# Performance work log

Hardware: AMD Instinct MI355X
Metric: run time of the kernel (lower is better)

## Reference

```python
import jax, jax.numpy as jnp
import numpy as np

N_NODES = 50000
N_EDGES = 800000
N_GRAPHS = 256
W_SCALE = 0.05  # keep activations bounded through 5 relu conv layers


def setup_inputs() -> dict:
    key = jax.random.key(0)
    ks = jax.random.split(key, 16)
    rn = lambda k, shape: W_SCALE * jax.random.normal(k, shape, dtype=jnp.float32)
    return {
        "x": jax.random.normal(ks[0], (N_NODES, 336), dtype=jnp.float32),
        "edge_index": jax.random.randint(ks[1], (2, N_EDGES), 0, N_NODES, dtype=jnp.int32),
        "batch": jnp.sort(jax.random.randint(ks[2], (N_NODES,), 0, N_GRAPHS, dtype=jnp.int32)),
        "w1_rel": rn(ks[3], (100, 336)),
        "w1_root": rn(ks[4], (100, 336)),
        "b1": rn(ks[5], (100,)),
        "w_rel": rn(ks[6], (4, 100, 100)),
        "w_root": rn(ks[7], (4, 100, 100)),
        "b": rn(ks[8], (4, 100)),
        "lw1": rn(ks[9], (100, 100)),
        "lb1": rn(ks[10], (100,)),
        "lw2": rn(ks[11], (100, 100)),
        "lb2": rn(ks[12], (100,)),
        "lw3": rn(ks[13], (29, 100)),
        "lb3": rn(ks[14], (29,)),
    }


def _graph_conv(x, edge_index, w_rel, w_root, bias):
    # PyG GraphConv: out_i = W_rel @ (sum_{j->i} x_j) + b + W_root @ x_i
    src, dst = edge_index[0], edge_index[1]
    agg = jax.ops.segment_sum(x[src], dst, num_segments=x.shape[0])  # [N, d_in]
    return agg @ w_rel.T + bias + x @ w_root.T


def reference(x, edge_index, batch, w1_rel, w1_root, b1, w_rel, w_root, b,
              lw1, lb1, lw2, lb2, lw3, lb3):
    h = jax.nn.relu(_graph_conv(x, edge_index, w1_rel, w1_root, b1))  # [N,100]
    for i in range(4):  # conv2..conv5 (structurally distinct params)
        h = jax.nn.relu(_graph_conv(h, edge_index, w_rel[i], w_root[i], b[i]))
    # global_mean_pool over graphs
    sums = jax.ops.segment_sum(h, batch, num_segments=N_GRAPHS)          # [G,100]
    counts = jax.ops.segment_sum(jnp.ones((h.shape[0],), h.dtype), batch,
                                 num_segments=N_GRAPHS)                  # [G]
    pooled = sums / jnp.maximum(counts, 1.0)[:, None]
    h = jax.nn.relu(pooled @ lw1.T + lb1)
    h = jax.nn.relu(h @ lw2.T + lb2)
    return h @ lw3.T + lb3  # [G, 29]
```

## Files before the change

### kernel.cpp

```cpp
#include <hip/hip_runtime.h>

#define N_NODES 50000
#define N_EDGES 800000
#define N_GRAPHS 256
#define F 100

#define SCAN_B 512
#define SCAN_NB 98
#define SCAN_PAD (SCAN_NB * SCAN_B)

#define PART_SZ 6250
#define FILL_CHUNK 2048
#define HIST_BLOCKS 3128

#define SROW 72
#define EPS 264
#define AST 264

#define SENT N_NODES
#define CSR_CAP 1155072

typedef __attribute__((ext_vector_type(8))) short bf16x8;
typedef __attribute__((ext_vector_type(4))) float f32x4;
typedef unsigned short ushort_t;
typedef unsigned int uint_t;

__device__ inline ushort_t f2bf(float f) {
  uint_t u = __float_as_uint(f);
  uint_t r = (u + 0x7fffu + ((u >> 16) & 1u)) >> 16;
  return (ushort_t)r;
}


__global__ __launch_bounds__(256) void pack_all(
    const float* __restrict__ w1_rel, const float* __restrict__ w1_root,
    const float* __restrict__ w_rel, const float* __restrict__ w_root,
    ushort_t* __restrict__ Wp1, ushort_t* __restrict__ Wf, int* __restrict__ cnt,
    int* __restrict__ csr, ushort_t* __restrict__ ZP,
    ushort_t* __restrict__ H1, ushort_t* __restrict__ H2) {
  int b = blockIdx.x;
  int tid = threadIdx.x;
  if (b < 208) {
    int row = b;
    for (int k = tid; k < 384; k += 256) {
      float v = 0.f;
      if (k < 336) {
        if (row < 100) v = w1_rel[row * 336 + k];
        else if (row < 200) v = w1_root[(row - 100) * 336 + k];
      }
      Wp1[(size_t)row * 384 + k] = f2bf(v);
    }
  } else if (b < 720) {
    int rowl = b - 208;
    int l = rowl >> 7, row = rowl & 127;
    int k = tid;
    float v = 0.f;
    if (row < 100) {
      if (k < 100) v = w_rel[((size_t)l * 100 + row) * 100 + k];
      else if (k >= 128 && k < 228) v = w_root[((size_t)l * 100 + row) * 100 + (k - 128)];
    }
    Wf[(size_t)rowl * 256 + k] = f2bf(v);
  } else if (b < 769) {
    int z = b - 720;
    *(int4*)(cnt + (size_t)z * 1024 + tid * 4) = make_int4(0, 0, 0, 0);
  } else if (b < 1051) {
    int i0 = (b - 769) * 4096 + tid * 16;
    int4 sv = make_int4(SENT, SENT, SENT, SENT);
    *(int4*)(csr + i0) = sv; *(int4*)(csr + i0 + 4) = sv;
    *(int4*)(csr + i0 + 8) = sv; *(int4*)(csr + i0 + 12) = sv;
  } else {
    uint4 z4 = make_uint4(0u, 0u, 0u, 0u);
    if (tid < 32)      *(uint4*)(ZP + (size_t)SENT * 256 + tid * 8) = z4;
    else if (tid < 48) *(uint4*)(H1 + (size_t)SENT * 128 + (tid - 32) * 8) = z4;
    else if (tid < 64) *(uint4*)(H2 + (size_t)SENT * 128 + (tid - 48) * 8) = z4;
  }
}


__global__ __launch_bounds__(256) void hist_kernel(const int* __restrict__ dst,
                                                   int* __restrict__ cnt, int E) {
  int part = blockIdx.x & 7;
  int lo = part * PART_SZ, hi = lo + PART_SZ;
  int base = (blockIdx.x >> 3) * FILL_CHUNK;
  int end = base + FILL_CHUNK; if (end > E) end = E;
  for (int i = base + threadIdx.x; i < end; i += 256) {
    int d = dst[i];
    if (d >= lo && d < hi) atomicAdd(&cnt[d], 1);
  }
}


__global__ __launch_bounds__(SCAN_B) void scan1_kernel(const int* __restrict__ cnt,
                                                       int* __restrict__ excl,
                                                       int* __restrict__ bsum) {
  __shared__ int sh[SCAN_B];
  int t = threadIdx.x;
  int i = blockIdx.x * SCAN_B + t;
  int v = (cnt[i] + 7) & ~7;
  sh[t] = v;
  __syncthreads();
  for (int off = 1; off < SCAN_B; off <<= 1) {
    int u = (t >= off) ? sh[t - off] : 0;
    __syncthreads();
    sh[t] += u;
    __syncthreads();
  }
  excl[i] = sh[t] - v;
  if (t == SCAN_B - 1) bsum[blockIdx.x] = sh[t];
}

__global__ __launch_bounds__(128) void scan2_kernel(int* __restrict__ bsum) {
  __shared__ int sh[128];
  int t = threadIdx.x;
  int v = (t < SCAN_NB) ? bsum[t] : 0;
  sh[t] = v;
  __syncthreads();
  for (int off = 1; off < 128; off <<= 1) {
    int u = (t >= off) ? sh[t - off] : 0;
    __syncthreads();
    sh[t] += u;
    __syncthreads();
  }
  if (t < SCAN_NB) bsum[t] = sh[t] - v;
}

__global__ __launch_bounds__(SCAN_B) void scan3_kernel(const int* __restrict__ excl,
                                                       const int* __restrict__ bsum,
                                                       int* __restrict__ offs,
                                                       int* __restrict__ cursor) {
  int i = blockIdx.x * SCAN_B + threadIdx.x;
  int v = excl[i] + bsum[blockIdx.x];
  if (i <= N_NODES) { offs[i] = v; cursor[i] = v; }
}


__global__ __launch_bounds__(256) void fill_kernel(const int* __restrict__ src,
                                                   const int* __restrict__ dst,
                                                   int* __restrict__ cursor,
                                                   int* __restrict__ csr_src, int E) {
  int part = blockIdx.x & 7;
  int lo = part * PART_SZ, hi = lo + PART_SZ;
  int base = (blockIdx.x >> 3) * FILL_CHUNK;
  int end = base + FILL_CHUNK; if (end > E) end = E;
  for (int i = base + threadIdx.x; i < end; i += 256) {
    int d = dst[i];
    if (d >= lo && d < hi) {
      int p = atomicAdd(&cursor[d], 1);
      csr_src[p] = src[i];
    }
  }
}


template <bool AF32>
__global__ __launch_bounds__(256) void conv_mfma(
    const void* __restrict__ Aptr, const ushort_t* __restrict__ Wp,
    const float* __restrict__ bias,
    ushort_t* __restrict__ ZP, int Kp) {
  __shared__ short smem[64 * SROW + 208 * SROW];
  __shared__ float bias_s[104];
  short* alds = smem;
  short* blds = smem + 64 * SROW;

  int tid = threadIdx.x;
  int n0 = blockIdx.x * 64;
  if (tid < 100) bias_s[tid] = bias[tid];

  f32x4 acc[13];
#pragma unroll
  for (int b = 0; b < 13; ++b) acc[b] = (f32x4)0.f;

  int w = tid >> 6, lane = tid & 63, q = lane >> 4, m16 = lane & 15;

  int ar[2], aq[2];
#pragma unroll
  for (int u = 0; u < 2; ++u) { int c = tid + u * 256; ar[u] = c >> 3; aq[u] = c & 7; }

  bf16x8 areg[2], breg[7];

  auto load_chunk = [&](int k0) {
#pragma unroll
    for (int u = 0; u < 2; ++u) {
      int node = n0 + ar[u];
      int k = k0 + aq[u] * 8;
      bf16x8 val = (bf16x8)0;
      if (AF32) {
        if (node < N_NODES && k < 336) {
          const float* p = (const float*)Aptr + (size_t)node * 336 + k;
          float4 f0 = *(const float4*)p;
          float4 f1 = *(const float4*)(p + 4);
          val[0] = (short)f2bf(f0.x); val[1] = (short)f2bf(f0.y);
          val[2] = (short)f2bf(f0.z); val[3] = (short)f2bf(f0.w);
          val[4] = (short)f2bf(f1.x); val[5] = (short)f2bf(f1.y);
          val[6] = (short)f2bf(f1.z); val[7] = (short)f2bf(f1.w);
        }
      } else {
        if (node < N_NODES)
          val = *(const bf16x8*)((const short*)Aptr + (size_t)node * 128 + k);
      }
      areg[u] = val;
    }
#pragma unroll
    for (int u = 0; u < 7; ++u) {
      int c = tid + u * 256;
      if (c < 1664) {
        int r = c >> 3, qq = c & 7;
        breg[u] = *(const bf16x8*)((const short*)Wp + (size_t)r * Kp + k0 + qq * 8);
      }
    }
  };

  load_chunk(0);

  for (int k0 = 0; k0 < Kp; k0 += 64) {
#pragma unroll
    for (int u = 0; u < 2; ++u)
      *(bf16x8*)&alds[ar[u] * SROW + aq[u] * 8] = areg[u];
#pragma unroll
    for (int u = 0; u < 7; ++u) {
      int c = tid + u * 256;
      if (c < 1664) {
        int r = c >> 3, qq = c & 7;
        *(bf16x8*)&blds[r * SROW + qq * 8] = breg[u];
      }
    }
    __syncthreads();
    if (k0 + 64 < Kp) load_chunk(k0 + 64);
#pragma unroll
    for (int s = 0; s < 2; ++s) {
      bf16x8 a = *(const bf16x8*)&alds[(w * 16 + m16) * SROW + s * 32 + q * 8];
#pragma unroll
      for (int b = 0; b < 13; ++b) {
        bf16x8 bf = *(const bf16x8*)&blds[(b * 16 + m16) * SROW + s * 32 + q * 8];
        acc[b] = __builtin_amdgcn_mfma_f32_16x16x32_bf16(a, bf, acc[b], 0, 0, 0);
      }
    }
    __syncthreads();
  }

  short* ep = smem;
#pragma unroll
  for (int b = 0; b < 13; ++b) {
    int n = b * 16 + m16;
    if (n < 200) {
      int c = (n < 100) ? n : (n + 28);
      float add = (n < 100) ? 0.f : bias_s[(n - 100) & 127];
#pragma unroll
      for (int r = 0; r < 4; ++r) {
        int row = w * 16 + q * 4 + r;
        ep[row * EPS + c] = (short)f2bf(acc[b][r] + add);
      }
    }
  }
  __syncthreads();
#pragma unroll
  for (int j = 0; j < 8; ++j) {
    int i = tid + j * 256;
    int row = i >> 5, c16 = i & 31;
    int node = n0 + row;
    if (node < N_NODES) {
      *(uint4*)(ZP + (size_t)node * 256 + c16 * 8) =
          *(const uint4*)&ep[row * EPS + c16 * 8];
    }
  }
}


__global__ __launch_bounds__(256) void gather_bf16(
    const ushort_t* __restrict__ ZP,
    const int* __restrict__ offs, const int* __restrict__ csr,
    ushort_t* __restrict__ H) {
  int lane = threadIdx.x & 63;
  int off = (lane < 50 ? lane : 49) * 2;
  int wid = threadIdx.x >> 6;
  int nA = __builtin_amdgcn_readfirstlane(blockIdx.x * 8 + wid * 2);
  int nB = nA + 1;

  uint_t zrA = *(const uint_t*)(ZP + (size_t)nA * 256 + 128 + off);
  uint_t zrB = *(const uint_t*)(ZP + (size_t)nB * 256 + 128 + off);

  int sA = offs[nA], sB = offs[nA + 1], eB = offs[nA + 2];
  int eA = sB;

  float pA0[8], pA1[8], pB0[8], pB1[8];
#pragma unroll
  for (int u = 0; u < 8; ++u) { pA0[u] = 0.f; pA1[u] = 0.f; pB0[u] = 0.f; pB1[u] = 0.f; }
  pA0[0] = __uint_as_float(zrA << 16);
  pA1[0] = __uint_as_float(zrA & 0xffff0000u);
  pB0[0] = __uint_as_float(zrB << 16);
  pB1[0] = __uint_as_float(zrB & 0xffff0000u);

  uint_t bA0[8], bA1[8], bB0[8], bB1[8];
  auto LD = [&](uint_t (&buf)[8], int vidx, int g) {
#pragma unroll
    for (int t = 0; t < 8; ++t) {
      int idx = __builtin_amdgcn_readlane(vidx, g * 8 + t);
      buf[t] = *(const uint_t*)(ZP + (size_t)idx * 256 + off);
    }
  };
  auto CS = [&](uint_t (&buf)[8], float (&p0)[8], float (&p1)[8]) {
#pragma unroll
    for (int t = 0; t < 8; ++t) {
      p0[t] += __uint_as_float(buf[t] << 16);
      p1[t] += __uint_as_float(buf[t] & 0xffff0000u);
    }
  };

  if (eA - sA <= 64 && eB - sB <= 64) {
    int ngA = (eA - sA) >> 3, ngB = (eB - sB) >> 3;
    int vA = csr[sA + lane];
    int vB = csr[sB + lane];
    if (ngA > 0) LD(bA0, vA, 0);
    if (ngB > 0) LD(bB0, vB, 0);
    int ngM = ngA > ngB ? ngA : ngB;
    for (int g = 0; g < ngM; g += 2) {
      if (g + 1 < ngA) LD(bA1, vA, g + 1);
      if (g + 1 < ngB) LD(bB1, vB, g + 1);
      if (g < ngA) CS(bA0, pA0, pA1);
      if (g < ngB) CS(bB0, pB0, pB1);
      if (g + 2 < ngA) LD(bA0, vA, g + 2);
      if (g + 2 < ngB) LD(bB0, vB, g + 2);
      if (g + 1 < ngA) CS(bA1, pA0, pA1);
      if (g + 1 < ngB) CS(bB1, pB0, pB1);
    }
  } else {
    auto seq = [&](int s, int e, float (&p0)[8], float (&p1)[8]) {
      for (int j = s; j < e; j += 64) {
        int rem = e - j;
        int ng = (rem > 64 ? 64 : rem) >> 3;
        int v = csr[j + lane];
        for (int g = 0; g < ng; ++g) { LD(bA0, v, g); CS(bA0, p0, p1); }
      }
    };
    seq(sA, eA, pA0, pA1);
    seq(sB, eB, pB0, pB1);
  }

  float a0 = ((pA0[0] + pA0[1]) + (pA0[2] + pA0[3])) + ((pA0[4] + pA0[5]) + (pA0[6] + pA0[7]));
  float a1 = ((pA1[0] + pA1[1]) + (pA1[2] + pA1[3])) + ((pA1[4] + pA1[5]) + (pA1[6] + pA1[7]));
  float b0 = ((pB0[0] + pB0[1]) + (pB0[2] + pB0[3])) + ((pB0[4] + pB0[5]) + (pB0[6] + pB0[7]));
  float b1 = ((pB1[0] + pB1[1]) + (pB1[2] + pB1[3])) + ((pB1[4] + pB1[5]) + (pB1[6] + pB1[7]));
  uint_t outA = (uint_t)f2bf(fmaxf(a0, 0.f)) | ((uint_t)f2bf(fmaxf(a1, 0.f)) << 16);
  uint_t outB = (uint_t)f2bf(fmaxf(b0, 0.f)) | ((uint_t)f2bf(fmaxf(b1, 0.f)) << 16);
  if (lane >= 50) { outA = 0u; outB = 0u; }
  *(uint_t*)(H + (size_t)nA * 128 + lane * 2) = outA;
  *(uint_t*)(H + (size_t)nB * 128 + lane * 2) = outB;
}


__global__ __launch_bounds__(512) void fused_layer(
    const ushort_t* __restrict__ Hin,
    const ushort_t* __restrict__ Wf,
    const float* __restrict__ bias,
    const int* __restrict__ offs, const int* __restrict__ csr,
    ushort_t* __restrict__ Hout) {
  __shared__ short alds[16 * AST];

  int tid = threadIdx.x;
  int w = tid >> 6, lane = tid & 63, q = lane >> 4, m16 = lane & 15;
  int tile = blockIdx.x;
  int off = (lane < 50 ? lane : 49) * 2;

  int rowA = w * 2, rowB = w * 2 + 1;
  int nA = __builtin_amdgcn_readfirstlane(tile * 16 + rowA);
  int nB = nA + 1;

  uint_t hvA = *(const uint_t*)(Hin + (size_t)nA * 128 + lane * 2);
  uint_t hvB = *(const uint_t*)(Hin + (size_t)nB * 128 + lane * 2);
  *(uint_t*)&alds[rowA * AST + 128 + lane * 2] = hvA;
  *(uint_t*)&alds[rowB * AST + 128 + lane * 2] = hvB;

  int sA = offs[nA], sB = offs[nA + 1], eB = offs[nA + 2];
  int eA = sB;

  float pA0[8], pA1[8], pB0[8], pB1[8];
#pragma unroll
  for (int u = 0; u < 8; ++u) { pA0[u] = 0.f; pA1[u] = 0.f; pB0[u] = 0.f; pB1[u] = 0.f; }

  uint_t bA0[8], bA1[8], bB0[8], bB1[8];
  auto LD = [&](uint_t (&buf)[8], int vidx, int g) {
#pragma unroll
    for (int t = 0; t < 8; ++t) {
      int idx = __builtin_amdgcn_readlane(vidx, g * 8 + t);
      buf[t] = *(const uint_t*)(Hin + (size_t)idx * 128 + off);
    }
  };
  auto CS = [&](uint_t (&buf)[8], float (&p0)[8], float (&p1)[8]) {
#pragma unroll
    for (int t = 0; t < 8; ++t) {
      p0[t] += __uint_as_float(buf[t] << 16);
      p1[t] += __uint_as_float(buf[t] & 0xffff0000u);
    }
  };

  if (eA - sA <= 64 && eB - sB <= 64) {
    int ngA = (eA - sA) >> 3, ngB = (eB - sB) >> 3;
    int vA = csr[sA + lane];
    int vB = csr[sB + lane];
    if (ngA > 0) LD(bA0, vA, 0);
    if (ngB > 0) LD(bB0, vB, 0);
    int ngM = ngA > ngB ? ngA : ngB;
    for (int g = 0; g < ngM; g += 2) {
      if (g + 1 < ngA) LD(bA1, vA, g + 1);
      if (g + 1 < ngB) LD(bB1, vB, g + 1);
      if (g < ngA) CS(bA0, pA0, pA1);
      if (g < ngB) CS(bB0, pB0, pB1);
      if (g + 2 < ngA) LD(bA0, vA, g + 2);
      if (g + 2 < ngB) LD(bB0, vB, g + 2);
      if (g + 1 < ngA) CS(bA1, pA0, pA1);
      if (g + 1 < ngB) CS(bB1, pB0, pB1);
    }
  } else {
    auto seq = [&](int s, int e, float (&p0)[8], float (&p1)[8]) {
      for (int j = s; j < e; j += 64) {
        int rem = e - j;
        int ng = (rem > 64 ? 64 : rem) >> 3;
        int v = csr[j + lane];
        for (int g = 0; g < ng; ++g) { LD(bA0, v, g); CS(bA0, p0, p1); }
      }
    };
    seq(sA, eA, pA0, pA1);
    seq(sB, eB, pB0, pB1);
  }

  float a0 = ((pA0[0] + pA0[1]) + (pA0[2] + pA0[3])) + ((pA0[4] + pA0[5]) + (pA0[6] + pA0[7]));
  float a1 = ((pA1[0] + pA1[1]) + (pA1[2] + pA1[3])) + ((pA1[4] + pA1[5]) + (pA1[6] + pA1[7]));
  float c0 = ((pB0[0] + pB0[1]) + (pB0[2] + pB0[3])) + ((pB0[4] + pB0[5]) + (pB0[6] + pB0[7]));
  float c1 = ((pB1[0] + pB1[1]) + (pB1[2] + pB1[3])) + ((pB1[4] + pB1[5]) + (pB1[6] + pB1[7]));
  uint_t outA = (uint_t)f2bf(a0) | ((uint_t)f2bf(a1) << 16);
  uint_t outB = (uint_t)f2bf(c0) | ((uint_t)f2bf(c1) << 16);
  if (lane >= 50) { outA = 0u; outB = 0u; }
  *(uint_t*)&alds[rowA * AST + lane * 2] = outA;
  *(uint_t*)&alds[rowB * AST + lane * 2] = outB;

  bf16x8 wreg[8];
#pragma unroll
  for (int s = 0; s < 8; ++s)
    wreg[s] = *(const bf16x8*)(Wf + (size_t)(w * 16 + m16) * 256 + s * 32 + q * 8);
  int n0 = w * 16 + q * 4;
  float4 bb = make_float4(0.f, 0.f, 0.f, 0.f);
  if (n0 < 100) bb = *(const float4*)(bias + n0);

  __syncthreads();
  f32x4 acc = (f32x4)0.f;
#pragma unroll
  for (int s = 0; s < 8; ++s) {
    bf16x8 af = *(const bf16x8*)&alds[m16 * AST + s * 32 + q * 8];
    acc = __builtin_amdgcn_mfma_f32_16x16x32_bf16(wreg[s], af, acc, 0, 0, 0);
  }
  int nodeo = tile * 16 + m16;
  ushort4 v;
  v.x = f2bf(fmaxf(acc[0] + bb.x, 0.f));
  v.y = f2bf(fmaxf(acc[1] + bb.y, 0.f));
  v.z = f2bf(fmaxf(acc[2] + bb.z, 0.f));
  v.w = f2bf(fmaxf(acc[3] + bb.w, 0.f));
  *(ushort4*)(Hout + (size_t)nodeo * 128 + n0) = v;
}


__global__ __launch_bounds__(1024) void pool_mlp(
    const ushort_t* __restrict__ H, const int* __restrict__ batch,
    const float* __restrict__ lw1, const float* __restrict__ lb1,
    const float* __restrict__ lw2, const float* __restrict__ lb2,
    const float* __restrict__ lw3, const float* __restrict__ lb3,
    float* __restrict__ out) {
  int g = blockIdx.x;
  int t = threadIdx.x;
  int lo = 0, hi = N_NODES;
  while (lo < hi) { int mid = (lo + hi) >> 1; if (batch[mid] < g) lo = mid + 1; else hi = mid; }
  int s = lo;
  hi = N_NODES;
  while (lo < hi) { int mid = (lo + hi) >> 1; if (batch[mid] <= g) lo = mid + 1; else hi = mid; }
  int e = lo;

  int row = t >> 6;
  int lane = t & 63;
  int off = (lane < 50 ? lane : 49) * 2;
  float a0 = 0.f, a1 = 0.f;
  for (int n = s + row; n < e; n += 16) {
    uint_t z = *(const uint_t*)(H + (size_t)n * 128 + off);
    a0 += __uint_as_float(z << 16);
    a1 += __uint_as_float(z & 0xffff0000u);
  }
  __shared__ float sh[16][104];
  __shared__ float r0[F], r1[F], r2[F];
  if (lane < 50) { sh[row][lane * 2] = a0; sh[row][lane * 2 + 1] = a1; }
  __syncthreads();
  if (t < F) {
    float acc = 0.f;
#pragma unroll
    for (int r = 0; r < 16; ++r) acc += sh[r][t];
    int cnt = e - s;
    float d = (cnt > 0) ? (float)cnt : 1.f;
    r0[t] = acc / d;
  }
  __syncthreads();
  if (t < F) {
    float sv = lb1[t];
    for (int k = 0; k < F; ++k) sv += r0[k] * lw1[t * F + k];
    r1[t] = fmaxf(sv, 0.f);
  }
  __syncthreads();
  if (t < F) {
    float sv = lb2[t];
    for (int k = 0; k < F; ++k) sv += r1[k] * lw2[t * F + k];
    r2[t] = fmaxf(sv, 0.f);
  }
  __syncthreads();
  if (t < 29) {
    float sv = lb3[t];
    for (int k = 0; k < F; ++k) sv += r2[k] * lw3[t * F + k];
    out[g * 29 + t] = sv;
  }
}


extern "C" void kernel_launch(void* const* d_in, const int* in_sizes, int n_in,
                              void* d_out, int out_size, void* d_ws, size_t ws_size,
                              hipStream_t stream) {
  const float* x       = (const float*)d_in[0];
  const int*   ei      = (const int*)d_in[1];
  const int*   batch   = (const int*)d_in[2];
  const float* w1_rel  = (const float*)d_in[3];
  const float* w1_root = (const float*)d_in[4];
  const float* b1      = (const float*)d_in[5];
  const float* w_rel   = (const float*)d_in[6];
  const float* w_root  = (const float*)d_in[7];
  const float* bvec    = (const float*)d_in[8];
  const float* lw1     = (const float*)d_in[9];
  const float* lb1     = (const float*)d_in[10];
  const float* lw2     = (const float*)d_in[11];
  const float* lb2     = (const float*)d_in[12];
  const float* lw3     = (const float*)d_in[13];
  const float* lb3     = (const float*)d_in[14];
  float* out = (float*)d_out;

  char* ws = (char*)d_ws;
  size_t o = 0;
  auto alloc = [&](size_t bytes) { void* p = ws + o; o = (o + bytes + 511) & ~(size_t)511; return p; };
  ushort_t* H1   = (ushort_t*)alloc((size_t)(N_NODES + 1) * 128 * 2);
  ushort_t* H2   = (ushort_t*)alloc((size_t)(N_NODES + 1) * 128 * 2);
  ushort_t* ZP   = (ushort_t*)alloc((size_t)(N_NODES + 1) * 256 * 2);
  ushort_t* Wp1  = (ushort_t*)alloc((size_t)208 * 384 * 2);
  ushort_t* Wf   = (ushort_t*)alloc((size_t)4 * 128 * 256 * 2);
  int* cnt    = (int*)alloc((size_t)SCAN_PAD * 4);
  int* excl   = (int*)alloc((size_t)SCAN_PAD * 4);
  int* bsum   = (int*)alloc((size_t)128 * 4);
  int* offs   = (int*)alloc((size_t)(N_NODES + 1) * 4);
  int* cursor = (int*)alloc((size_t)(N_NODES + 1) * 4);
  int* csr    = (int*)alloc((size_t)CSR_CAP * 4);

  const int E = N_EDGES;
  const int* srcv = ei;
  const int* dstv = ei + E;

  pack_all<<<1052, 256, 0, stream>>>(w1_rel, w1_root, w_rel, w_root, Wp1, Wf, cnt, csr, ZP, H1, H2);
  hist_kernel<<<HIST_BLOCKS, 256, 0, stream>>>(dstv, cnt, E);
  scan1_kernel<<<SCAN_NB, SCAN_B, 0, stream>>>(cnt, excl, bsum);
  scan2_kernel<<<1, 128, 0, stream>>>(bsum);
  scan3_kernel<<<SCAN_NB, SCAN_B, 0, stream>>>(excl, bsum, offs, cursor);
  fill_kernel<<<HIST_BLOCKS, 256, 0, stream>>>(srcv, dstv, cursor, csr, E);

  int mmgrid = (N_NODES + 63) / 64;
  conv_mfma<true><<<mmgrid, 256, 0, stream>>>(x, Wp1, b1, ZP, 384);
  gather_bf16<<<N_NODES / 8, 256, 0, stream>>>(ZP, offs, csr, H1);

  const ushort_t* hin = H1;
  ushort_t* hout = H2;
  for (int l = 0; l < 4; ++l) {
    fused_layer<<<N_NODES / 16, 512, 0, stream>>>(hin, Wf + (size_t)l * 128 * 256,
                                                  bvec + (size_t)l * F, offs, csr, hout);
    const ushort_t* tmp = hout; hout = (ushort_t*)hin; hin = tmp;
  }
  pool_mlp<<<N_GRAPHS, 1024, 0, stream>>>(hin, batch, lw1, lb1, lw2, lb2, lw3, lb3, out);
}
```

Before: 462.4 us.

## Stream contiguous CSR edge ranges per wave across 16 destination nodes

Replaces the per-node-pair gather (readlane index broadcast, per-node loops) with a streaming gather where each wave walks the contiguous CSR range of 16 consecutive destinations. Edge indices are loaded as int4 vectors and double-buffered, and partial sums are flushed whenever a node boundary is crossed. The fused layer now processes 64 nodes per 256-thread block and computes all 128 output columns per wave, staging the results through LDS for coalesced stores. This aims to balance work across nodes of uneven degree and cut per-node overhead. It relies on the CSR being padded to multiples of 8 (SENT entries), and it adds zero-init of the epilogue LDS in conv_mfma.

```diff
diff --git a/kernel.cpp b/kernel.cpp
--- a/kernel.cpp
+++ b/kernel.cpp
@@ -15,7 +15,7 @@
 
 #define SROW 72
 #define EPS 264
-#define AST 264
+#define AST2 272
 
 #define SENT N_NODES
 #define CSR_CAP 1155072
@@ -240,6 +240,12 @@
 
   short* ep = smem;
 #pragma unroll
+  for (int j = 0; j < 9; ++j) {
+    int i = tid + j * 256;
+    if (i < 64 * EPS / 8) *(uint4*)&ep[i * 8] = make_uint4(0u, 0u, 0u, 0u);
+  }
+  __syncthreads();
+#pragma unroll
   for (int b = 0; b < 13; ++b) {
     int n = b * 16 + m16;
     if (n < 200) {
@@ -266,195 +272,179 @@
 }
 
 
-__global__ __launch_bounds__(256) void gather_bf16(
+__global__ __launch_bounds__(256) void gather_stream(
     const ushort_t* __restrict__ ZP,
     const int* __restrict__ offs, const int* __restrict__ csr,
     ushort_t* __restrict__ H) {
   int lane = threadIdx.x & 63;
-  int off = (lane < 50 ? lane : 49) * 2;
   int wid = threadIdx.x >> 6;
-  int nA = __builtin_amdgcn_readfirstlane(blockIdx.x * 8 + wid * 2);
-  int nB = nA + 1;
-
-  uint_t zrA = *(const uint_t*)(ZP + (size_t)nA * 256 + 128 + off);
-  uint_t zrB = *(const uint_t*)(ZP + (size_t)nB * 256 + 128 + off);
-
-  int sA = offs[nA], sB = offs[nA + 1], eB = offs[nA + 2];
-  int eA = sB;
-
-  float pA0[8], pA1[8], pB0[8], pB1[8];
-#pragma unroll
-  for (int u = 0; u < 8; ++u) { pA0[u] = 0.f; pA1[u] = 0.f; pB0[u] = 0.f; pB1[u] = 0.f; }
-  pA0[0] = __uint_as_float(zrA << 16);
-  pA1[0] = __uint_as_float(zrA & 0xffff0000u);
-  pB0[0] = __uint_as_float(zrB << 16);
-  pB1[0] = __uint_as_float(zrB & 0xffff0000u);
-
-  uint_t bA0[8], bA1[8], bB0[8], bB1[8];
-  auto LD = [&](uint_t (&buf)[8], int vidx, int g) {
+  int d0 = __builtin_amdgcn_readfirstlane(blockIdx.x * 64 + wid * 16);
+  if (d0 >= N_NODES) return;
+  int dlim = d0 + 16; if (dlim > N_NODES) dlim = N_NODES;
+  int offc = (lane < 50 ? lane : 49) * 2;
+
+  float p0 = 0.f, p1 = 0.f;
+  int d = d0;
+
+  auto flushd = [&](int dd, float a0, float a1) {
+    uint_t zr = *(const uint_t*)(ZP + (size_t)dd * 256 + 128 + offc);
+    a0 += __uint_as_float(zr << 16);
+    a1 += __uint_as_float(zr & 0xffff0000u);
+    a0 = fmaxf(a0, 0.f); a1 = fmaxf(a1, 0.f);
+    uint_t o = (uint_t)f2bf(a0) | ((uint_t)f2bf(a1) << 16);
+    if (lane >= 50) o = 0u;
+    *(uint_t*)(H + (size_t)dd * 128 + lane * 2) = o;
+  };
+
+  int s0 = offs[d0], e0 = offs[dlim];
+  int nextoff = offs[d + 1];
+  uint_t bA[8], bB[8];
+  auto issue = [&](uint_t (&buf)[8], int i) {
+    int4 sa = *(const int4*)(csr + i);
+    int4 sb = *(const int4*)(csr + i + 4);
+    buf[0] = *(const uint_t*)(ZP + (size_t)sa.x * 256 + offc);
+    buf[1] = *(const uint_t*)(ZP + (size_t)sa.y * 256 + offc);
+    buf[2] = *(const uint_t*)(ZP + (size_t)sa.z * 256 + offc);
+    buf[3] = *(const uint_t*)(ZP + (size_t)sa.w * 256 + offc);
+    buf[4] = *(const uint_t*)(ZP + (size_t)sb.x * 256 + offc);
+    buf[5] = *(const uint_t*)(ZP + (size_t)sb.y * 256 + offc);
+    buf[6] = *(const uint_t*)(ZP + (size_t)sb.z * 256 + offc);
+    buf[7] = *(const uint_t*)(ZP + (size_t)sb.w * 256 + offc);
+  };
+  auto cons = [&](uint_t (&buf)[8]) {
 #pragma unroll
     for (int t = 0; t < 8; ++t) {
-      int idx = __builtin_amdgcn_readlane(vidx, g * 8 + t);
-      buf[t] = *(const uint_t*)(ZP + (size_t)idx * 256 + off);
+      p0 += __uint_as_float(buf[t] << 16);
+      p1 += __uint_as_float(buf[t] & 0xffff0000u);
     }
   };
-  auto CS = [&](uint_t (&buf)[8], float (&p0)[8], float (&p1)[8]) {
-#pragma unroll
-    for (int t = 0; t < 8; ++t) {
-      p0[t] += __uint_as_float(buf[t] << 16);
-      p1[t] += __uint_as_float(buf[t] & 0xffff0000u);
-    }
-  };
-
-  if (eA - sA <= 64 && eB - sB <= 64) {
-    int ngA = (eA - sA) >> 3, ngB = (eB - sB) >> 3;
-    int vA = csr[sA + lane];
-    int vB = csr[sB + lane];
-    if (ngA > 0) LD(bA0, vA, 0);
-    if (ngB > 0) LD(bB0, vB, 0);
-    int ngM = ngA > ngB ? ngA : ngB;
-    for (int g = 0; g < ngM; g += 2) {
-      if (g + 1 < ngA) LD(bA1, vA, g + 1);
-      if (g + 1 < ngB) LD(bB1, vB, g + 1);
-      if (g < ngA) CS(bA0, pA0, pA1);
-      if (g < ngB) CS(bB0, pB0, pB1);
-      if (g + 2 < ngA) LD(bA0, vA, g + 2);
-      if (g + 2 < ngB) LD(bB0, vB, g + 2);
-      if (g + 1 < ngA) CS(bA1, pA0, pA1);
-      if (g + 1 < ngB) CS(bB1, pB0, pB1);
-    }
-  } else {
-    auto seq = [&](int s, int e, float (&p0)[8], float (&p1)[8]) {
-      for (int j = s; j < e; j += 64) {
-        int rem = e - j;
-        int ng = (rem > 64 ? 64 : rem) >> 3;
-        int v = csr[j + lane];
-        for (int g = 0; g < ng; ++g) { LD(bA0, v, g); CS(bA0, p0, p1); }
-      }
-    };
-    seq(sA, eA, pA0, pA1);
-    seq(sB, eB, pB0, pB1);
-  }
-
-  float a0 = ((pA0[0] + pA0[1]) + (pA0[2] + pA0[3])) + ((pA0[4] + pA0[5]) + (pA0[6] + pA0[7]));
-  float a1 = ((pA1[0] + pA1[1]) + (pA1[2] + pA1[3])) + ((pA1[4] + pA1[5]) + (pA1[6] + pA1[7]));
-  float b0 = ((pB0[0] + pB0[1]) + (pB0[2] + pB0[3])) + ((pB0[4] + pB0[5]) + (pB0[6] + pB0[7]));
-  float b1 = ((pB1[0] + pB1[1]) + (pB1[2] + pB1[3])) + ((pB1[4] + pB1[5]) + (pB1[6] + pB1[7]));
-  uint_t outA = (uint_t)f2bf(fmaxf(a0, 0.f)) | ((uint_t)f2bf(fmaxf(a1, 0.f)) << 16);
-  uint_t outB = (uint_t)f2bf(fmaxf(b0, 0.f)) | ((uint_t)f2bf(fmaxf(b1, 0.f)) << 16);
-  if (lane >= 50) { outA = 0u; outB = 0u; }
-  *(uint_t*)(H + (size_t)nA * 128 + lane * 2) = outA;
-  *(uint_t*)(H + (size_t)nB * 128 + lane * 2) = outB;
-}
-
-
-__global__ __launch_bounds__(512) void fused_layer(
+
+  int i = s0;
+  if (i < e0) issue(bA, i);
+  while (i < e0) {
+    if (i + 8 < e0) issue(bB, i + 8);
+    while (i == nextoff) { flushd(d, p0, p1); p0 = 0.f; p1 = 0.f; ++d; nextoff = offs[d + 1]; }
+    cons(bA);
+    i += 8;
+    if (i >= e0) break;
+    if (i + 8 < e0) issue(bA, i + 8);
+    while (i == nextoff) { flushd(d, p0, p1); p0 = 0.f; p1 = 0.f; ++d; nextoff = offs[d + 1]; }
+    cons(bB);
+    i += 8;
+  }
+  while (d < dlim) { flushd(d, p0, p1); p0 = 0.f; p1 = 0.f; ++d; }
+}
+
+
+__global__ __launch_bounds__(256) void fused_stream(
     const ushort_t* __restrict__ Hin,
     const ushort_t* __restrict__ Wf,
     const float* __restrict__ bias,
     const int* __restrict__ offs, const int* __restrict__ csr,
     ushort_t* __restrict__ Hout) {
-  __shared__ short alds[16 * AST];
+  __shared__ short alds[64 * AST2];
+  __shared__ __align__(16) float bias_s[128];
 
   int tid = threadIdx.x;
-  int w = tid >> 6, lane = tid & 63, q = lane >> 4, m16 = lane & 15;
-  int tile = blockIdx.x;
-  int off = (lane < 50 ? lane : 49) * 2;
-
-  int rowA = w * 2, rowB = w * 2 + 1;
-  int nA = __builtin_amdgcn_readfirstlane(tile * 16 + rowA);
-  int nB = nA + 1;
-
-  uint_t hvA = *(const uint_t*)(Hin + (size_t)nA * 128 + lane * 2);
-  uint_t hvB = *(const uint_t*)(Hin + (size_t)nB * 128 + lane * 2);
-  *(uint_t*)&alds[rowA * AST + 128 + lane * 2] = hvA;
-  *(uint_t*)&alds[rowB * AST + 128 + lane * 2] = hvB;
-
-  int sA = offs[nA], sB = offs[nA + 1], eB = offs[nA + 2];
-  int eA = sB;
-
-  float pA0[8], pA1[8], pB0[8], pB1[8];
-#pragma unroll
-  for (int u = 0; u < 8; ++u) { pA0[u] = 0.f; pA1[u] = 0.f; pB0[u] = 0.f; pB1[u] = 0.f; }
-
-  uint_t bA0[8], bA1[8], bB0[8], bB1[8];
-  auto LD = [&](uint_t (&buf)[8], int vidx, int g) {
-#pragma unroll
-    for (int t = 0; t < 8; ++t) {
-      int idx = __builtin_amdgcn_readlane(vidx, g * 8 + t);
-      buf[t] = *(const uint_t*)(Hin + (size_t)idx * 128 + off);
-    }
+  int lane = tid & 63, wid = tid >> 6;
+  int q = lane >> 4, m16 = lane & 15;
+  if (tid < 128) bias_s[tid] = (tid < 100) ? bias[tid] : 0.f;
+
+  int bd0 = blockIdx.x * 64;
+  int d0 = __builtin_amdgcn_readfirstlane(bd0 + wid * 16);
+
+  float p0 = 0.f, p1 = 0.f;
+  auto flushA = [&](int dd, float a0, float a1) {
+    uint_t o = (uint_t)f2bf(a0) | ((uint_t)f2bf(a1) << 16);
+    *(uint_t*)&alds[(dd - bd0) * AST2 + lane * 2] = o;
   };
-  auto CS = [&](uint_t (&buf)[8], float (&p0)[8], float (&p1)[8]) {
-#pragma unroll
-    for (int t = 0; t < 8; ++t) {
-      p0[t] += __uint_as_float(buf[t] << 16);
-      p1[t] += __uint_as_float(buf[t] & 0xffff0000u);
-    }
-  };
-
-  if (eA - sA <= 64 && eB - sB <= 64) {
-    int ngA = (eA - sA) >> 3, ngB = (eB - sB) >> 3;
-    int vA = csr[sA + lane];
-    int vB = csr[sB + lane];
-    if (ngA > 0) LD(bA0, vA, 0);
-    if (ngB > 0) LD(bB0, vB, 0);
-    int ngM = ngA > ngB ? ngA : ngB;
-    for (int g = 0; g < ngM; g += 2) {
-      if (g + 1 < ngA) LD(bA1, vA, g + 1);
-      if (g + 1 < ngB) LD(bB1, vB, g + 1);
-      if (g < ngA) CS(bA0, pA0, pA1);
-      if (g < ngB) CS(bB0, pB0, pB1);
-      if (g + 2 < ngA) LD(bA0, vA, g + 2);
-      if (g + 2 < ngB) LD(bB0, vB, g + 2);
-      if (g + 1 < ngA) CS(bA1, pA0, pA1);
-      if (g + 1 < ngB) CS(bB1, pB0, pB1);
-    }
+
+  if (d0 < N_NODES) {
+    int dlim = d0 + 16; if (dlim > N_NODES) dlim = N_NODES;
+    int s0 = offs[d0], e0 = offs[dlim];
+    int d = d0;
+    int nextoff = offs[d + 1];
+    uint_t bA[8], bB[8];
+    auto issue = [&](uint_t (&buf)[8], int i) {
+      int4 sa = *(const int4*)(csr + i);
+      int4 sb = *(const int4*)(csr + i + 4);
+      buf[0] = *(const uint_t*)(Hin + (size_t)sa.x * 128 + lane * 2);
+      buf[1] = *(const uint_t*)(Hin + (size_t)sa.y * 128 + lane * 2);
+      buf[2] = *(const uint_t*)(Hin + (size_t)sa.z * 128 + lane * 2);
+      buf[3] = *(const uint_t*)(Hin + (size_t)sa.w * 128 + lane * 2);
+      buf[4] = *(const uint_t*)(Hin + (size_t)sb.x * 128 + lane * 2);
+      buf[5] = *(const uint_t*)(Hin + (size_t)sb.y * 128 + lane * 2);
+      buf[6] = *(const uint_t*)(Hin + (size_t)sb.z * 128 + lane * 2);
+      buf[7] = *(const uint_t*)(Hin + (size_t)sb.w * 128 + lane * 2);
+    };
+    auto cons = [&](uint_t (&buf)[8]) {
+#pragma unroll
+      for (int t = 0; t < 8; ++t) {
+        p0 += __uint_as_float(buf[t] << 16);
+        p1 += __uint_as_float(buf[t] & 0xffff0000u);
+      }
+    };
+    int i = s0;
+    if (i < e0) issue(bA, i);
+    while (i < e0) {
+      if (i + 8 < e0) issue(bB, i + 8);
+      while (i == nextoff) { flushA(d, p0, p1); p0 = 0.f; p1 = 0.f; ++d; nextoff = offs[d + 1]; }
+      cons(bA);
+      i += 8;
+      if (i >= e0) break;
+      if (i + 8 < e0) issue(bA, i + 8);
+      while (i == nextoff) { flushA(d, p0, p1); p0 = 0.f; p1 = 0.f; ++d; nextoff = offs[d + 1]; }
+      cons(bB);
+      i += 8;
+    }
+    while (d < d0 + 16) { flushA(d, p0, p1); p0 = 0.f; p1 = 0.f; ++d; }
   } else {
-    auto seq = [&](int s, int e, float (&p0)[8], float (&p1)[8]) {
-      for (int j = s; j < e; j += 64) {
-        int rem = e - j;
-        int ng = (rem > 64 ? 64 : rem) >> 3;
-        int v = csr[j + lane];
-        for (int g = 0; g < ng; ++g) { LD(bA0, v, g); CS(bA0, p0, p1); }
-      }
-    };
-    seq(sA, eA, pA0, pA1);
-    seq(sB, eB, pB0, pB1);
-  }
-
-  float a0 = ((pA0[0] + pA0[1]) + (pA0[2] + pA0[3])) + ((pA0[4] + pA0[5]) + (pA0[6] + pA0[7]));
-  float a1 = ((pA1[0] + pA1[1]) + (pA1[2] + pA1[3])) + ((pA1[4] + pA1[5]) + (pA1[6] + pA1[7]));
-  float c0 = ((pB0[0] + pB0[1]) + (pB0[2] + pB0[3])) + ((pB0[4] + pB0[5]) + (pB0[6] + pB0[7]));
-  float c1 = ((pB1[0] + pB1[1]) + (pB1[2] + pB1[3])) + ((pB1[4] + pB1[5]) + (pB1[6] + pB1[7]));
-  uint_t outA = (uint_t)f2bf(a0) | ((uint_t)f2bf(a1) << 16);
-  uint_t outB = (uint_t)f2bf(c0) | ((uint_t)f2bf(c1) << 16);
-  if (lane >= 50) { outA = 0u; outB = 0u; }
-  *(uint_t*)&alds[rowA * AST + lane * 2] = outA;
-  *(uint_t*)&alds[rowB * AST + lane * 2] = outB;
-
-  bf16x8 wreg[8];
-#pragma unroll
-  for (int s = 0; s < 8; ++s)
-    wreg[s] = *(const bf16x8*)(Wf + (size_t)(w * 16 + m16) * 256 + s * 32 + q * 8);
-  int n0 = w * 16 + q * 4;
-  float4 bb = make_float4(0.f, 0.f, 0.f, 0.f);
-  if (n0 < 100) bb = *(const float4*)(bias + n0);
-
-  __syncthreads();
-  f32x4 acc = (f32x4)0.f;
-#pragma unroll
-  for (int s = 0; s < 8; ++s) {
-    bf16x8 af = *(const bf16x8*)&alds[m16 * AST + s * 32 + q * 8];
-    acc = __builtin_amdgcn_mfma_f32_16x16x32_bf16(wreg[s], af, acc, 0, 0, 0);
-  }
-  int nodeo = tile * 16 + m16;
-  ushort4 v;
-  v.x = f2bf(fmaxf(acc[0] + bb.x, 0.f));
-  v.y = f2bf(fmaxf(acc[1] + bb.y, 0.f));
-  v.z = f2bf(fmaxf(acc[2] + bb.z, 0.f));
-  v.w = f2bf(fmaxf(acc[3] + bb.w, 0.f));
-  *(ushort4*)(Hout + (size_t)nodeo * 128 + n0) = v;
+    for (int dd = d0; dd < d0 + 16; ++dd) flushA(dd, 0.f, 0.f);
+  }
+
+  for (int r = 0; r < 16; ++r) {
+    int dd = d0 + r;
+    int srcrow = (dd < N_NODES) ? dd : SENT;
+    uint_t hv = *(const uint_t*)(Hin + (size_t)srcrow * 128 + lane * 2);
+    *(uint_t*)&alds[(dd - bd0) * AST2 + 128 + lane * 2] = hv;
+  }
+  __syncthreads();
+
+  f32x4 acc[8];
+#pragma unroll
+  for (int wb = 0; wb < 8; ++wb) acc[wb] = (f32x4)0.f;
+#pragma unroll
+  for (int kb = 0; kb < 8; ++kb) {
+    bf16x8 af = *(const bf16x8*)&alds[(wid * 16 + m16) * AST2 + kb * 32 + q * 8];
+#pragma unroll
+    for (int wb = 0; wb < 8; ++wb) {
+      bf16x8 wf = *(const bf16x8*)(Wf + (size_t)(wb * 16 + m16) * 256 + kb * 32 + q * 8);
+      acc[wb] = __builtin_amdgcn_mfma_f32_16x16x32_bf16(wf, af, acc[wb], 0, 0, 0);
+    }
+  }
+  __syncthreads();
+
+#pragma unroll
+  for (int wb = 0; wb < 8; ++wb) {
+    int col0 = wb * 16 + q * 4;
+    float4 bb = *(const float4*)&bias_s[col0];
+    ushort4 v;
+    v.x = f2bf(fmaxf(acc[wb][0] + bb.x, 0.f));
+    v.y = f2bf(fmaxf(acc[wb][1] + bb.y, 0.f));
+    v.z = f2bf(fmaxf(acc[wb][2] + bb.z, 0.f));
+    v.w = f2bf(fmaxf(acc[wb][3] + bb.w, 0.f));
+    *(ushort4*)&alds[(wid * 16 + m16) * AST2 + col0] = v;
+  }
+  __syncthreads();
+
+#pragma unroll
+  for (int j = 0; j < 4; ++j) {
+    int i2 = tid + j * 256;
+    int row = i2 >> 4, c = i2 & 15;
+    int node = bd0 + row;
+    if (node < N_NODES)
+      *(uint4*)(Hout + (size_t)node * 128 + c * 8) = *(const uint4*)&alds[row * AST2 + c * 8];
+  }
 }
 
 
@@ -538,8 +528,8 @@
   char* ws = (char*)d_ws;
   size_t o = 0;
   auto alloc = [&](size_t bytes) { void* p = ws + o; o = (o + bytes + 511) & ~(size_t)511; return p; };
-  ushort_t* H1   = (ushort_t*)alloc((size_t)(N_NODES + 1) * 128 * 2);
-  ushort_t* H2   = (ushort_t*)alloc((size_t)(N_NODES + 1) * 128 * 2);
+  ushort_t* H1   = (ushort_t*)alloc((size_t)(N_NODES + 64) * 128 * 2);
+  ushort_t* H2   = (ushort_t*)alloc((size_t)(N_NODES + 64) * 128 * 2);
   ushort_t* ZP   = (ushort_t*)alloc((size_t)(N_NODES + 1) * 256 * 2);
   ushort_t* Wp1  = (ushort_t*)alloc((size_t)208 * 384 * 2);
   ushort_t* Wf   = (ushort_t*)alloc((size_t)4 * 128 * 256 * 2);
@@ -563,13 +553,13 @@
 
   int mmgrid = (N_NODES + 63) / 64;
   conv_mfma<true><<<mmgrid, 256, 0, stream>>>(x, Wp1, b1, ZP, 384);
-  gather_bf16<<<N_NODES / 8, 256, 0, stream>>>(ZP, offs, csr, H1);
+  gather_stream<<<(N_NODES + 63) / 64, 256, 0, stream>>>(ZP, offs, csr, H1);
 
   const ushort_t* hin = H1;
   ushort_t* hout = H2;
   for (int l = 0; l < 4; ++l) {
-    fused_layer<<<N_NODES / 16, 512, 0, stream>>>(hin, Wf + (size_t)l * 128 * 256,
-                                                  bvec + (size_t)l * F, offs, csr, hout);
+    fused_stream<<<(N_NODES + 63) / 64, 256, 0, stream>>>(hin, Wf + (size_t)l * 128 * 256,
+                                                          bvec + (size_t)l * F, offs, csr, hout);
     const ushort_t* tmp = hout; hout = (ushort_t*)hin; hin = tmp;
   }
   pool_mlp<<<N_GRAPHS, 1024, 0, stream>>>(hin, batch, lw1, lb1, lw2, lb2, lw3, lb3, out);
```

Result: slower. 507.4 us (+9.7%).
